# Optimization experiments

Measured on AMD Instinct MI355X. Metric: run time of the kernel, lower is better.

Reference implementation:

```python
import jax, jax.numpy as jnp
import numpy as np

D_MODEL = 1024
H = 16
D_K = D_MODEL // H


def setup_inputs() -> dict:
    key = jax.random.key(0)
    ks = jax.random.split(key, 11)
    B, S = 4, 2048
    q = jax.random.normal(ks[0], (B, S, D_MODEL), dtype=jnp.float32)
    k = jax.random.normal(ks[1], (B, S, D_MODEL), dtype=jnp.float32)
    v = jax.random.normal(ks[2], (B, S, D_MODEL), dtype=jnp.float32)
    mask = jnp.ones((1, 1, S, S), dtype=bool)  # all-ones = no masking
    scale = 1.0 / np.sqrt(D_MODEL)
    wq = jax.random.normal(ks[3], (D_MODEL, D_MODEL), dtype=jnp.float32) * scale
    wk = jax.random.normal(ks[4], (D_MODEL, D_MODEL), dtype=jnp.float32) * scale
    wv = jax.random.normal(ks[5], (D_MODEL, D_MODEL), dtype=jnp.float32) * scale
    wo = jax.random.normal(ks[6], (D_MODEL, D_MODEL), dtype=jnp.float32) * scale
    bq = jnp.zeros((D_MODEL,), jnp.float32)
    bk = jnp.zeros((D_MODEL,), jnp.float32)
    bv = jnp.zeros((D_MODEL,), jnp.float32)
    bo = jnp.zeros((D_MODEL,), jnp.float32)
    return {"q": q, "k": k, "v": v, "mask": mask,
            "wq": wq, "bq": bq, "wk": wk, "bk": bk,
            "wv": wv, "bv": bv, "wo": wo, "bo": bo}


def reference(q, k, v, mask, wq, bq, wk, bk, wv, bv, wo, bo):
    B, S, _ = q.shape
    # projections (Linear uses x @ W^T + b)
    qh = (q @ wq.T + bq).reshape(B, S, H, D_K).transpose(0, 2, 1, 3)  # [B,H,S,Dk]
    kh = (k @ wk.T + bk).reshape(B, S, H, D_K).transpose(0, 2, 1, 3)
    vh = (v @ wv.T + bv).reshape(B, S, H, D_K).transpose(0, 2, 1, 3)
    scores = jnp.einsum("bhqd,bhkd->bhqk", qh, kh) / jnp.sqrt(jnp.float32(D_K))
    scores = jnp.where(mask, scores, jnp.float32(-1e9))
    attn = jax.nn.softmax(scores, axis=-1)  # dropout p=0.0 -> identity
    out = jnp.einsum("bhqk,bhkd->bhqd", attn, vh)  # [B,H,S,Dk]
    out = out.transpose(0, 2, 1, 3).reshape(B, S, D_MODEL)
    return out @ wo.T + bo
```

## Files before the change

kernel.cpp:

```cpp
#include <hip/hip_runtime.h>
#include <hip/hip_bf16.h>


typedef __attribute__((ext_vector_type(8))) short bf16x8;
typedef __attribute__((ext_vector_type(4))) float f32x4;
typedef __attribute__((ext_vector_type(16))) float f32x16;

__device__ __forceinline__ float fast_exp2(float x) {
  return __builtin_amdgcn_exp2f(x);
}

__device__ __forceinline__ void gload_lds16(const void* g, void* l) {
  __builtin_amdgcn_global_load_lds(
      (const __attribute__((address_space(1))) unsigned int*)g,
      (__attribute__((address_space(3))) unsigned int*)l, 16, 0, 0);
}

__global__ void cvt_bf16_multi(const float* __restrict__ s0, const float* __restrict__ s1,
                               const float* __restrict__ s2, const float* __restrict__ s3,
                               __hip_bfloat16* __restrict__ d0, __hip_bfloat16* __restrict__ d1,
                               __hip_bfloat16* __restrict__ d2, __hip_bfloat16* __restrict__ d3,
                               int n4) {
  const int z = blockIdx.y;
  const float* in = (z == 0) ? s0 : (z == 1) ? s1 : (z == 2) ? s2 : s3;
  __hip_bfloat16* out = (z == 0) ? d0 : (z == 1) ? d1 : (z == 2) ? d2 : d3;
  int stride = gridDim.x * blockDim.x;
  for (int i = blockIdx.x * blockDim.x + threadIdx.x; i < n4; i += stride) {
    float4 f = reinterpret_cast<const float4*>(in)[i];
    union { __hip_bfloat16 h[4]; ushort4 u; } cv;
    cv.h[0] = __float2bfloat16(f.x);
    cv.h[1] = __float2bfloat16(f.y);
    cv.h[2] = __float2bfloat16(f.z);
    cv.h[3] = __float2bfloat16(f.w);
    reinterpret_cast<ushort4*>(out)[i] = cv.u;
  }
}

template <int MODE, int ASRC>
__device__ __forceinline__ void gemm_tile(const void* Av,
                                          const __hip_bfloat16* __restrict__ W,
                                          const float* __restrict__ bias,
                                          void* __restrict__ out, float scale,
                                          int m0, int n0,
                                          __hip_bfloat16* As, __hip_bfloat16* Bs) {
  const int t = threadIdx.x;
  const int lane = t & 63;
  const int w = t >> 6;
  const int lrow = lane & 15, lk = lane >> 4;
  const int wr = (w >> 1) << 6;
  const int wc = (w & 1) << 6;
  const int K = 1024, N = 1024;

  f32x4 acc[4][4] = {};
  const char* Ab = (const char*)As;
  const char* Bb = (const char*)Bs;

  for (int kt = 0; kt < K; kt += 64) {
    #pragma unroll
    for (int j = 0; j < 4; ++j) {
      int i = j * 256 + t;
      int row = i >> 3;
      int cs = ((i & 7) ^ (row & 7)) << 3;
      gload_lds16(W + (size_t)(n0 + row) * K + kt + cs, (char*)Bs + (i << 4));
      if (ASRC == 0)
        gload_lds16((const __hip_bfloat16*)Av + (size_t)(m0 + row) * K + kt + cs,
                    (char*)As + (i << 4));
    }
    if (ASRC == 1) {
      const float* A32 = (const float*)Av;
      #pragma unroll
      for (int j = 0; j < 4; ++j) {
        int i = j * 256 + t;
        int row = i >> 3;
        int cs = ((i & 7) ^ (row & 7)) << 3;
        const float* src = A32 + (size_t)(m0 + row) * K + kt + cs;
        float4 f0 = *(const float4*)src;
        float4 f1 = *(const float4*)(src + 4);
        union { __hip_bfloat16 h[8]; bf16x8 v; } cv;
        cv.h[0] = __float2bfloat16(f0.x);
        cv.h[1] = __float2bfloat16(f0.y);
        cv.h[2] = __float2bfloat16(f0.z);
        cv.h[3] = __float2bfloat16(f0.w);
        cv.h[4] = __float2bfloat16(f1.x);
        cv.h[5] = __float2bfloat16(f1.y);
        cv.h[6] = __float2bfloat16(f1.z);
        cv.h[7] = __float2bfloat16(f1.w);
        *(bf16x8*)((char*)As + (i << 4)) = cv.v;
      }
    }
    __syncthreads();
    #pragma unroll
    for (int h = 0; h < 2; ++h) {
      bf16x8 a[4], b[4];
      #pragma unroll
      for (int f = 0; f < 4; ++f) {
        const int sw = ((h * 4 + lk) ^ (lrow & 7)) << 4;
        a[f] = *(const bf16x8*)(Ab + (wr + f * 16 + lrow) * 128 + sw);
        b[f] = *(const bf16x8*)(Bb + (wc + f * 16 + lrow) * 128 + sw);
      }
      #pragma unroll
      for (int fi = 0; fi < 4; ++fi)
        #pragma unroll
        for (int fj = 0; fj < 4; ++fj)
          acc[fi][fj] = __builtin_amdgcn_mfma_f32_16x16x32_bf16(a[fi], b[fj], acc[fi][fj], 0, 0, 0);
    }
    __syncthreads();
  }

  #pragma unroll
  for (int fi = 0; fi < 4; ++fi) {
    int rbase = m0 + wr + fi * 16 + (lk << 2);
    #pragma unroll
    for (int fj = 0; fj < 4; ++fj) {
      int gc = n0 + wc + fj * 16 + lrow;
      float bv = bias[gc];
      #pragma unroll
      for (int r = 0; r < 4; ++r) {
        int gm = rbase + r;
        float val = (acc[fi][fj][r] + bv) * scale;
        if (MODE == 0) {
          int bb = gm >> 11, ss = gm & 2047, hh = gc >> 6, dd = gc & 63;
          ((__hip_bfloat16*)out)[((((size_t)bb * 16 + hh) * 2048 + ss) << 6) + dd] =
              __float2bfloat16(val);
        } else {
          ((float*)out)[(size_t)gm * N + gc] = val;
        }
      }
    }
  }
}

__global__ __launch_bounds__(256, 3)
void gemm_qkv_kernel(const float* __restrict__ A0, const float* __restrict__ A1,
                     const float* __restrict__ A2,
                     const __hip_bfloat16* __restrict__ W0, const __hip_bfloat16* __restrict__ W1,
                     const __hip_bfloat16* __restrict__ W2,
                     const float* __restrict__ b0, const float* __restrict__ b1,
                     const float* __restrict__ b2,
                     __hip_bfloat16* __restrict__ o0, __hip_bfloat16* __restrict__ o1,
                     __hip_bfloat16* __restrict__ o2,
                     float sc0, float sc1, float sc2) {
  __shared__ __hip_bfloat16 As[128 * 64];
  __shared__ __hip_bfloat16 Bs[128 * 64];
  const int flat = blockIdx.x;
  const int swz = (flat & 7) * 192 + (flat >> 3);
  const int z = swz >> 9;
  const int rem = swz & 511;
  const int m0 = (rem >> 3) << 7;
  const int n0 = (rem & 7) << 7;
  const float* A = A0; const __hip_bfloat16* W = W0;
  const float* bias = b0; __hip_bfloat16* out = o0; float scale = sc0;
  if (z == 1) { A = A1; W = W1; bias = b1; out = o1; scale = sc1; }
  else if (z == 2) { A = A2; W = W2; bias = b2; out = o2; scale = sc2; }
  gemm_tile<0, 1>(A, W, bias, out, scale, m0, n0, As, Bs);
}

__global__ __launch_bounds__(256, 3)
void gemm_out_kernel(const __hip_bfloat16* __restrict__ A, const __hip_bfloat16* __restrict__ W,
                     const float* __restrict__ bias, float* __restrict__ out) {
  __shared__ __hip_bfloat16 As[128 * 64];
  __shared__ __hip_bfloat16 Bs[128 * 64];
  const int flat = blockIdx.x;
  const int swz = (flat & 7) * 64 + (flat >> 3);
  const int m0 = (swz >> 3) << 7;
  const int n0 = (swz & 7) << 7;
  gemm_tile<1, 0>(A, W, bias, out, 1.0f, m0, n0, As, Bs);
}


template <int OFF>
__device__ __forceinline__ bf16x8 pack8(const f32x16& v) {
  bf16x8 r;
  #pragma unroll
  for (int e = 0; e < 8; ++e) {
    union { __hip_bfloat16 h; short s; } u;
    u.h = __float2bfloat16(v[OFF + e]);
    r[e] = u.s;
  }
  return r;
}

__global__ __launch_bounds__(512, 4)
void attn32_kernel(const __hip_bfloat16* __restrict__ qh,
                   const __hip_bfloat16* __restrict__ kh,
                   const __hip_bfloat16* __restrict__ vh,
                   __hip_bfloat16* __restrict__ att) {
  const int t = threadIdx.x;
  const int lane = t & 63, w = t >> 6;
  const int l31 = lane & 31, g = lane >> 5;
  const int bh = blockIdx.x, q0 = blockIdx.y << 8;

  const __hip_bfloat16* Qp = qh + (size_t)bh * 2048 * 64;
  const __hip_bfloat16* Kp = kh + (size_t)bh * 2048 * 64;
  const __hip_bfloat16* Vp = vh + (size_t)bh * 2048 * 64;

  __shared__ __align__(16) char lds[4 * 8192 + 4 * 9216];
  char* const Vbase = lds + 4 * 8192;

  const int qrow = q0 + w * 32 + l31;
  bf16x8 bq[4];
  #pragma unroll
  for (int ks = 0; ks < 4; ++ks)
    bq[ks] = *(const bf16x8*)(Qp + (size_t)qrow * 64 + ks * 16 + g * 8);

  f32x16 o0 = {}, o1 = {};
  float m_run = -1e30f, l_run = 0.f;

  const int krow = t >> 3, kcc = t & 7;
  const size_t kgo = (size_t)krow * 64 + ((kcc ^ (krow & 7)) << 3);
  const int klo = t << 4;
  const int vkey = t & 63, vdb = (t >> 6) << 3;
  const size_t vgo = (size_t)vkey * 64 + vdb;
  const int kpos = (vkey & 0x30) | (vkey & 3) | ((vkey & 4) << 1) | ((vkey & 8) >> 1);
  int ka[4], kb_[4], va_[4], vb_[4];
  #pragma unroll
  for (int ks = 0; ks < 4; ++ks) {
    ka[ks] = l31 * 128 + (((ks * 2 + g) ^ (l31 & 7)) << 4);
    kb_[ks] = ka[ks] + 32 * 128;
  }
  #pragma unroll
  for (int st = 0; st < 4; ++st) {
    va_[st] = l31 * 144 + st * 32 + g * 16;
    vb_[st] = va_[st] + 32 * 144;
  }

  auto vwrite = [&](char* Vn, const bf16x8& v) {
    #pragma unroll
    for (int e = 0; e < 8; ++e)
      *(unsigned short*)(Vn + (vdb + e) * 144 + kpos * 2) = (unsigned short)v[e];
  };

  auto subtile = [&](const char* Kc, const char* Vc) {
    f32x16 s0 = {}, s1 = {};
    __builtin_amdgcn_s_setprio(1);
    #pragma unroll
    for (int ks = 0; ks < 4; ++ks) {
      bf16x8 a0 = *(const bf16x8*)(Kc + ka[ks]);
      bf16x8 a1 = *(const bf16x8*)(Kc + kb_[ks]);
      s0 = __builtin_amdgcn_mfma_f32_32x32x16_bf16(a0, bq[ks], s0, 0, 0, 0);
      s1 = __builtin_amdgcn_mfma_f32_32x32x16_bf16(a1, bq[ks], s1, 0, 0, 0);
    }
    __builtin_amdgcn_s_setprio(0);

    float mx[8];
    #pragma unroll
    for (int j = 0; j < 8; ++j)
      mx[j] = fmaxf(fmaxf(s0[j], s0[j + 8]), fmaxf(s1[j], s1[j + 8]));
    float tm = fmaxf(fmaxf(fmaxf(mx[0], mx[1]), fmaxf(mx[2], mx[3])),
                     fmaxf(fmaxf(mx[4], mx[5]), fmaxf(mx[6], mx[7])));
    tm = fmaxf(tm, __shfl_xor(tm, 32));
    if (!__all(tm <= m_run + 11.5416f)) {
      float mn = fmaxf(m_run, tm);
      float sc = fast_exp2(m_run - mn);
      m_run = mn; l_run *= sc;
      #pragma unroll
      for (int j = 0; j < 16; ++j) { o0[j] *= sc; o1[j] *= sc; }
    }
    #pragma unroll
    for (int j = 0; j < 16; ++j) {
      s0[j] = fast_exp2(s0[j] - m_run);
      s1[j] = fast_exp2(s1[j] - m_run);
    }
    float as[8];
    #pragma unroll
    for (int j = 0; j < 8; ++j) as[j] = (s0[j] + s0[j + 8]) + (s1[j] + s1[j + 8]);
    float ps = ((as[0] + as[1]) + (as[2] + as[3])) + ((as[4] + as[5]) + (as[6] + as[7]));
    ps += __shfl_xor(ps, 32);
    l_run += ps;

    bf16x8 pb0 = pack8<0>(s0), pb1 = pack8<8>(s0);
    bf16x8 pb2 = pack8<0>(s1), pb3 = pack8<8>(s1);

    __builtin_amdgcn_s_setprio(1);
    #pragma unroll
    for (int st = 0; st < 4; ++st) {
      bf16x8 av0 = *(const bf16x8*)(Vc + va_[st]);
      bf16x8 av1 = *(const bf16x8*)(Vc + vb_[st]);
      const bf16x8 pb = (st == 0) ? pb0 : (st == 1) ? pb1 : (st == 2) ? pb2 : pb3;
      o0 = __builtin_amdgcn_mfma_f32_32x32x16_bf16(av0, pb, o0, 0, 0, 0);
      o1 = __builtin_amdgcn_mfma_f32_32x32x16_bf16(av1, pb, o1, 0, 0, 0);
    }
    __builtin_amdgcn_s_setprio(0);
  };

  {
    #pragma unroll
    for (int s = 0; s < 2; ++s) {
      gload_lds16(Kp + s * 4096 + kgo, lds + s * 8192 + klo);
      bf16x8 v0 = *(const bf16x8*)(Vp + s * 4096 + vgo);
      vwrite(Vbase + s * 9216, v0);
    }
  }
  __syncthreads();

  for (int it = 0; it < 16; ++it) {
    const int P = it & 1;
    const char* Kc0 = lds + (P * 2) * 8192;
    const char* Kc1 = Kc0 + 8192;
    const char* Vc0 = Vbase + (P * 2) * 9216;
    const char* Vc1 = Vc0 + 9216;
    char* Kn0 = lds + ((P ^ 1) * 2) * 8192;
    char* Vn0 = Vbase + ((P ^ 1) * 2) * 9216;

    bf16x8 vrA, vrB;
    const bool pre = (it < 15);
    if (pre) {
      const size_t nb = (size_t)(it + 1) * 8192;
      gload_lds16(Kp + nb + kgo, Kn0 + klo);
      gload_lds16(Kp + nb + 4096 + kgo, Kn0 + 8192 + klo);
      vrA = *(const bf16x8*)(Vp + nb + vgo);
      vrB = *(const bf16x8*)(Vp + nb + 4096 + vgo);
    }

    subtile(Kc0, Vc0);
    subtile(Kc1, Vc1);

    if (pre) {
      vwrite(Vn0, vrA);
      vwrite(Vn0 + 9216, vrB);
    }
    __syncthreads();
  }

  const int bb = bh >> 4, hh = bh & 15;
  const float inv = 1.f / l_run;
  __hip_bfloat16* obase = att + ((size_t)bb * 2048 + qrow) * 1024 + hh * 64 + g * 16;

  auto epi = [&](const f32x16& acc, __hip_bfloat16* dst) {
    float fin[16];
    #pragma unroll
    for (int c2 = 0; c2 < 2; ++c2)
      #pragma unroll
      for (int c4 = 0; c4 < 4; ++c4) {
        float sendv = g ? acc[c4 + 4 * c2] : acc[c4 + 4 * (2 + c2)];
        float recvv = __shfl_xor(sendv, 32);
        float ownv  = g ? acc[c4 + 4 * (2 + c2)] : acc[c4 + 4 * c2];
        fin[c2 * 8 + c4]     = g ? recvv : ownv;
        fin[c2 * 8 + 4 + c4] = g ? ownv : recvv;
      }
    bf16x8 w0, w1;
    #pragma unroll
    for (int j = 0; j < 8; ++j) {
      union { __hip_bfloat16 h; short s; } u0, u1;
      u0.h = __float2bfloat16(fin[j] * inv);
      u1.h = __float2bfloat16(fin[8 + j] * inv);
      w0[j] = u0.s; w1[j] = u1.s;
    }
    *(bf16x8*)dst = w0;
    *(bf16x8*)(dst + 8) = w1;
  };
  epi(o0, obase);
  epi(o1, obase + 32);
}

extern "C" void kernel_launch(void* const* d_in, const int* in_sizes, int n_in,
                              void* d_out, int out_size, void* d_ws, size_t ws_size,
                              hipStream_t stream) {
  (void)in_sizes; (void)n_in; (void)out_size; (void)ws_size;
  const float* q  = (const float*)d_in[0];
  const float* k  = (const float*)d_in[1];
  const float* v  = (const float*)d_in[2];
  const float* wq = (const float*)d_in[4];
  const float* bq = (const float*)d_in[5];
  const float* wk = (const float*)d_in[6];
  const float* bk = (const float*)d_in[7];
  const float* wv = (const float*)d_in[8];
  const float* bv = (const float*)d_in[9];
  const float* wo = (const float*)d_in[10];
  const float* bo = (const float*)d_in[11];

  char* ws = (char*)d_ws;
  const size_t MB = 1u << 20;
  __hip_bfloat16* wqb  = (__hip_bfloat16*)(ws);
  __hip_bfloat16* wkb  = (__hip_bfloat16*)(ws + 2 * MB);
  __hip_bfloat16* wvb  = (__hip_bfloat16*)(ws + 4 * MB);
  __hip_bfloat16* wob  = (__hip_bfloat16*)(ws + 6 * MB);
  __hip_bfloat16* qhb  = (__hip_bfloat16*)(ws + 8 * MB);
  __hip_bfloat16* khb  = (__hip_bfloat16*)(ws + 24 * MB);
  __hip_bfloat16* vhb  = (__hip_bfloat16*)(ws + 40 * MB);
  __hip_bfloat16* attb = (__hip_bfloat16*)(ws + 56 * MB);

  dim3 blk(256);
  const int nw4 = (1024 * 1024) / 4;
  const float qscale = 0.125f * 1.44269504f;

  cvt_bf16_multi<<<dim3(256, 4), blk, 0, stream>>>(wq, wk, wv, wo,
                                                   wqb, wkb, wvb, wob, nw4);

  gemm_qkv_kernel<<<dim3(1536), blk, 0, stream>>>(q, k, v, wqb, wkb, wvb,
                                                  bq, bk, bv, qhb, khb, vhb,
                                                  qscale, 1.0f, 1.0f);

  attn32_kernel<<<dim3(64, 8), dim3(512), 0, stream>>>(qhb, khb, vhb, attb);

  gemm_out_kernel<<<dim3(512), blk, 0, stream>>>(attb, wob, bo, (float*)d_out);
}
```

Measured before the change: 193.2 us.

## Prefetch next GEMM K-tile into registers while computing current tile

Replaces the direct global-to-LDS loads with register staging. The next K-tile of A and W is loaded into registers before the MFMA loop on the current tile, then written to LDS at the top of the next iteration. The aim is to overlap global memory latency with compute, at the cost of more VGPRs (float4 staging for the fp32 A path) and losing the async global_load_lds path for the bf16 operands.

```diff
diff --git a/kernel.cpp b/kernel.cpp
--- a/kernel.cpp
+++ b/kernel.cpp
@@ -55,40 +55,55 @@
   const char* Ab = (const char*)As;
   const char* Bb = (const char*)Bs;
 
-  for (int kt = 0; kt < K; kt += 64) {
+  float4 fa[4][2];
+  bf16x8 ab[4];
+  bf16x8 wb[4];
+
+  auto loadRegs = [&](int kt) {
     #pragma unroll
     for (int j = 0; j < 4; ++j) {
       int i = j * 256 + t;
       int row = i >> 3;
       int cs = ((i & 7) ^ (row & 7)) << 3;
-      gload_lds16(W + (size_t)(n0 + row) * K + kt + cs, (char*)Bs + (i << 4));
-      if (ASRC == 0)
-        gload_lds16((const __hip_bfloat16*)Av + (size_t)(m0 + row) * K + kt + cs,
-                    (char*)As + (i << 4));
-    }
-    if (ASRC == 1) {
-      const float* A32 = (const float*)Av;
-      #pragma unroll
-      for (int j = 0; j < 4; ++j) {
-        int i = j * 256 + t;
-        int row = i >> 3;
-        int cs = ((i & 7) ^ (row & 7)) << 3;
-        const float* src = A32 + (size_t)(m0 + row) * K + kt + cs;
-        float4 f0 = *(const float4*)src;
-        float4 f1 = *(const float4*)(src + 4);
+      if (ASRC == 1) {
+        const float* src = (const float*)Av + (size_t)(m0 + row) * K + kt + cs;
+        fa[j][0] = *(const float4*)src;
+        fa[j][1] = *(const float4*)(src + 4);
+      } else {
+        ab[j] = *(const bf16x8*)((const __hip_bfloat16*)Av +
+                                 (size_t)(m0 + row) * K + kt + cs);
+      }
+      wb[j] = *(const bf16x8*)(W + (size_t)(n0 + row) * K + kt + cs);
+    }
+  };
+
+  auto writeLDS = [&]() {
+    #pragma unroll
+    for (int j = 0; j < 4; ++j) {
+      int i = j * 256 + t;
+      if (ASRC == 1) {
         union { __hip_bfloat16 h[8]; bf16x8 v; } cv;
-        cv.h[0] = __float2bfloat16(f0.x);
-        cv.h[1] = __float2bfloat16(f0.y);
-        cv.h[2] = __float2bfloat16(f0.z);
-        cv.h[3] = __float2bfloat16(f0.w);
-        cv.h[4] = __float2bfloat16(f1.x);
-        cv.h[5] = __float2bfloat16(f1.y);
-        cv.h[6] = __float2bfloat16(f1.z);
-        cv.h[7] = __float2bfloat16(f1.w);
+        cv.h[0] = __float2bfloat16(fa[j][0].x);
+        cv.h[1] = __float2bfloat16(fa[j][0].y);
+        cv.h[2] = __float2bfloat16(fa[j][0].z);
+        cv.h[3] = __float2bfloat16(fa[j][0].w);
+        cv.h[4] = __float2bfloat16(fa[j][1].x);
+        cv.h[5] = __float2bfloat16(fa[j][1].y);
+        cv.h[6] = __float2bfloat16(fa[j][1].z);
+        cv.h[7] = __float2bfloat16(fa[j][1].w);
         *(bf16x8*)((char*)As + (i << 4)) = cv.v;
+      } else {
+        *(bf16x8*)((char*)As + (i << 4)) = ab[j];
       }
-    }
+      *(bf16x8*)((char*)Bs + (i << 4)) = wb[j];
+    }
+  };
+
+  loadRegs(0);
+  for (int kt = 0; kt < K; kt += 64) {
+    writeLDS();
     __syncthreads();
+    if (kt + 64 < K) loadRegs(kt + 64);
     #pragma unroll
     for (int h = 0; h < 2; ++h) {
       bf16x8 a[4], b[4];
```

Result: no change. 193.3 us (+0.1%).
